# Kernel tuning notes

Hardware: AMD Instinct MI355X
Metric: run time of the kernel (lower is better)

Reference implementation:

```python
import jax, jax.numpy as jnp
import numpy as np

N, D, H, OUT, B = 100000, 512, 1024, 250, 256
EPS = 1e-5


def layernorm(x, g, b):
    m = jnp.mean(x, axis=-1, keepdims=True)
    v = jnp.mean(jnp.square(x - m), axis=-1, keepdims=True)
    return (x - m) * jax.lax.rsqrt(v + EPS) * g + b


def setup_inputs() -> dict:
    key = jax.random.key(0)
    ks = jax.random.split(key, 10)
    s = lambda fan: (2.0 / fan) ** 0.5  # kaiming-ish scale
    return {
        "x": jax.random.normal(ks[0], (N, D), jnp.float32),
        "batch_ids": jnp.sort(jax.random.randint(ks[1], (N,), 0, B)),
        "gW1": jax.random.normal(ks[2], (2 * D, D), jnp.float32) * s(D),
        "gb1": jnp.zeros((2 * D,), jnp.float32),
        "gln_g": jnp.ones((2 * D,), jnp.float32),
        "gln_b": jnp.zeros((2 * D,), jnp.float32),
        "gW2": jax.random.normal(ks[3], (1, 2 * D), jnp.float32) * s(2 * D),
        "gb2": jnp.zeros((1,), jnp.float32),
        "pn_g": jnp.ones((D,), jnp.float32),
        "pn_b": jnp.zeros((D,), jnp.float32),
        "mW1": jax.random.normal(ks[4], (H, D), jnp.float32) * s(D),
        "mb1": jnp.zeros((H,), jnp.float32),
        "mln_g": jnp.ones((H,), jnp.float32),
        "mln_b": jnp.zeros((H,), jnp.float32),
        "mW2": jax.random.normal(ks[5], (OUT, H), jnp.float32) * s(H),
        "mb2": jnp.zeros((OUT,), jnp.float32),
    }


def reference(x, batch_ids, gW1, gb1, gln_g, gln_b, gW2, gb2,
              pn_g, pn_b, mW1, mb1, mln_g, mln_b, mW2, mb2):
    # gate MLP: Linear -> LayerNorm -> ReLU -> Linear(->1)
    h = jax.nn.relu(layernorm(x @ gW1.T + gb1, gln_g, gln_b))  # [N, 2D]
    gate = (h @ gW2.T + gb2)[:, 0]                              # [N]
    # segment-wise softmax over batch_ids
    seg_max = jax.ops.segment_max(gate, batch_ids, num_segments=B)
    e = jnp.exp(gate - jax.lax.stop_gradient(seg_max)[batch_ids])
    denom = jax.ops.segment_sum(e, batch_ids, num_segments=B)
    w = e / denom[batch_ids]                                    # [N]
    pooled = jax.ops.segment_sum(w[:, None] * x, batch_ids, num_segments=B)  # [B, D]
    out = layernorm(pooled, pn_g, pn_b)
    # classifier MLP (dropout = identity in eval)
    z = jax.nn.relu(layernorm(out @ mW1.T + mb1, mln_g, mln_b))
    logits = z @ mW2.T + mb2                                    # [B, OUT]
    return logits
```

## Files before the change

### kernel.cpp

```cpp
#include <hip/hip_runtime.h>
#include <stdint.h>

typedef unsigned int u32;
typedef unsigned short u16;

#define NROWS 100000
#define DIM 512
#define HDIM 1024
#define OUTF 250
#define NSEG 256
#define LNEPS 1e-5f
#define BM 32
#define NG 3125

typedef __bf16 bf16_t;
typedef bf16_t bf16x4 __attribute__((ext_vector_type(4)));
typedef bf16_t bf16x8 __attribute__((ext_vector_type(8)));
typedef float f32x4 __attribute__((ext_vector_type(4)));

__device__ inline int lower_bound(const int* __restrict__ a, int n, int v) {
    int lo = 0, hi = n;
    while (lo < hi) {
        int m = (lo + hi) >> 1;
        if (a[m] < v) lo = m + 1; else hi = m;
    }
    return lo;
}

__global__ __launch_bounds__(256) void k_conv(const float* __restrict__ gW1,
                                              const float* __restrict__ mW1,
                                              const float* __restrict__ mW2,
                                              u16* __restrict__ Wf,
                                              u16* __restrict__ mW1f,
                                              u16* __restrict__ mW2f) {
    int bid = blockIdx.x;
    if (bid < 512) {
        const float* src_base = (bid < 256) ? gW1 : mW1;
        u16* dst = (bid < 256) ? Wf : mW1f;
        int gid  = (bid & 255) * 256 + threadIdx.x;
        int lane = gid & 63;
        int grp  = gid >> 6;
        int ks   = grp >> 6, nt = grp & 63;
        int n    = nt * 16 + (lane & 15);
        int k0   = ks * 32 + ((lane >> 4) << 3);
        const float* src = src_base + (size_t)n * DIM + k0;
        float4 f0 = *reinterpret_cast<const float4*>(src);
        float4 f1 = *reinterpret_cast<const float4*>(src + 4);
        bf16x8 v;
        v[0] = (bf16_t)f0.x; v[1] = (bf16_t)f0.y;
        v[2] = (bf16_t)f0.z; v[3] = (bf16_t)f0.w;
        v[4] = (bf16_t)f1.x; v[5] = (bf16_t)f1.y;
        v[6] = (bf16_t)f1.z; v[7] = (bf16_t)f1.w;
        reinterpret_cast<bf16x8*>(dst)[gid] = v;
    } else {
        int gid  = (bid - 512) * 256 + threadIdx.x;
        int lane = gid & 63;
        int grp  = gid >> 6;
        int ks   = grp >> 4, nt = grp & 15;
        int n    = nt * 16 + (lane & 15);
        int k0   = ks * 32 + ((lane >> 4) << 3);
        bf16x8 v;
        if (n < OUTF) {
            const float* src = mW2 + (size_t)n * HDIM + k0;
            float4 f0 = *reinterpret_cast<const float4*>(src);
            float4 f1 = *reinterpret_cast<const float4*>(src + 4);
            v[0] = (bf16_t)f0.x; v[1] = (bf16_t)f0.y;
            v[2] = (bf16_t)f0.z; v[3] = (bf16_t)f0.w;
            v[4] = (bf16_t)f1.x; v[5] = (bf16_t)f1.y;
            v[6] = (bf16_t)f1.z; v[7] = (bf16_t)f1.w;
        } else {
            #pragma unroll
            for (int j = 0; j < 8; ++j) v[j] = (bf16_t)0.f;
        }
        reinterpret_cast<bf16x8*>(mW2f)[gid] = v;
    }
}

__global__ __launch_bounds__(512) void k_gate(
    const float* __restrict__ x, const u16* __restrict__ Wf,
    const float* __restrict__ gb1,
    const float* __restrict__ gln_g, const float* __restrict__ gln_b,
    const float* __restrict__ gW2, const float* __restrict__ gb2,
    float* __restrict__ gate)
{
    __shared__ __align__(16) u16 xlds[BM * DIM];
    __shared__ float redS[8][BM];
    __shared__ float redQ[8][BM];
    __shared__ float meanA[BM], rstdA[BM];

    const int tid  = threadIdx.x;
    const int lane = tid & 63;
    const int w    = tid >> 6;
    const int l15  = lane & 15;
    const int g4   = lane >> 4;
    const int row0 = blockIdx.x * BM;

    #pragma unroll
    for (int uu = 0; uu < 4; ++uu) {
        int lu  = uu * 512 + tid;
        int r   = lu >> 6;
        int u   = lu & 63;
        const float* src = x + (size_t)(row0 + r) * DIM + (u << 3);
        float4 f0 = *reinterpret_cast<const float4*>(src);
        float4 f1 = *reinterpret_cast<const float4*>(src + 4);
        bf16x8 v;
        v[0] = (bf16_t)f0.x; v[1] = (bf16_t)f0.y;
        v[2] = (bf16_t)f0.z; v[3] = (bf16_t)f0.w;
        v[4] = (bf16_t)f1.x; v[5] = (bf16_t)f1.y;
        v[6] = (bf16_t)f1.z; v[7] = (bf16_t)f1.w;
        int phys = r * DIM + ((u ^ (r & 7)) << 3);
        *reinterpret_cast<bf16x8*>(&xlds[phys]) = v;
    }
    __syncthreads();

    f32x4 acc[2][8];
    #pragma unroll
    for (int m = 0; m < 2; ++m)
        #pragma unroll
        for (int t = 0; t < 8; ++t)
            acc[m][t] = (f32x4){0.f, 0.f, 0.f, 0.f};

    const bf16x8* __restrict__ WfB = reinterpret_cast<const bf16x8*>(Wf);

    auto loadB = [&](bf16x8 (&b)[8], int ks) {
        #pragma unroll
        for (int t = 0; t < 8; ++t)
            b[t] = WfB[(ks * 64 + w * 8 + t) * 64 + lane];
    };
    auto loadA = [&](bf16x8 (&a)[2], int ks) {
        #pragma unroll
        for (int m = 0; m < 2; ++m) {
            int r = m * 16 + l15;
            int u = ks * 4 + g4;
            a[m] = *reinterpret_cast<const bf16x8*>(&xlds[r * DIM + ((u ^ (r & 7)) << 3)]);
        }
    };
    auto domfma = [&](bf16x8 (&a)[2], bf16x8 (&b)[8]) {
        #pragma unroll
        for (int m = 0; m < 2; ++m)
            #pragma unroll
            for (int t = 0; t < 8; ++t)
                acc[m][t] = __builtin_amdgcn_mfma_f32_16x16x32_bf16(a[m], b[t], acc[m][t], 0, 0, 0);
    };

    bf16x8 b0[8], b1[8], a0[2], a1[2];
    loadB(b0, 0); loadA(a0, 0);
    #pragma unroll
    for (int ks2 = 0; ks2 < 8; ++ks2) {
        loadB(b1, 2 * ks2 + 1);
        loadA(a1, 2 * ks2 + 1);
        domfma(a0, b0);
        if (ks2 < 7) {
            loadB(b0, 2 * ks2 + 2);
            loadA(a0, 2 * ks2 + 2);
        }
        domfma(a1, b1);
    }

    float cbias[8];
    #pragma unroll
    for (int t = 0; t < 8; ++t) cbias[t] = gb1[(w * 8 + t) * 16 + l15];
    #pragma unroll
    for (int m = 0; m < 2; ++m)
        #pragma unroll
        for (int t = 0; t < 8; ++t)
            #pragma unroll
            for (int j = 0; j < 4; ++j)
                acc[m][t][j] += cbias[t];

    #pragma unroll
    for (int m = 0; m < 2; ++m) {
        #pragma unroll
        for (int j = 0; j < 4; ++j) {
            float s1 = 0.f, s2 = 0.f;
            #pragma unroll
            for (int t = 0; t < 8; ++t) {
                float v = acc[m][t][j];
                s1 += v; s2 += v * v;
            }
            #pragma unroll
            for (int off = 1; off < 16; off <<= 1) {
                s1 += __shfl_xor(s1, off);
                s2 += __shfl_xor(s2, off);
            }
            if (l15 == 0) {
                int row = m * 16 + g4 * 4 + j;
                redS[w][row] = s1;
                redQ[w][row] = s2;
            }
        }
    }
    __syncthreads();
    if (tid < BM) {
        float S1 = 0.f, S2 = 0.f;
        #pragma unroll
        for (int ww = 0; ww < 8; ++ww) { S1 += redS[ww][tid]; S2 += redQ[ww][tid]; }
        float mean = S1 * (1.0f / 1024.0f);
        float var  = S2 * (1.0f / 1024.0f) - mean * mean;
        meanA[tid] = mean;
        rstdA[tid] = rsqrtf(var + LNEPS);
    }
    __syncthreads();

    float cg[8], cb[8], cw[8];
    #pragma unroll
    for (int t = 0; t < 8; ++t) {
        int c = (w * 8 + t) * 16 + l15;
        cg[t] = gln_g[c]; cb[t] = gln_b[c]; cw[t] = gW2[c];
    }
    #pragma unroll
    for (int m = 0; m < 2; ++m) {
        #pragma unroll
        for (int j = 0; j < 4; ++j) {
            int row = m * 16 + g4 * 4 + j;
            float mn = meanA[row];
            float rs = rstdA[row];
            float gp = 0.f;
            #pragma unroll
            for (int t = 0; t < 8; ++t) {
                float h = (acc[m][t][j] - mn) * rs * cg[t] + cb[t];
                gp += fmaxf(h, 0.f) * cw[t];
            }
            #pragma unroll
            for (int off = 1; off < 16; off <<= 1)
                gp += __shfl_xor(gp, off);
            if (l15 == 0) redS[w][row] = gp;
        }
    }
    __syncthreads();
    if (tid < BM) {
        float s = gb2[0];
        #pragma unroll
        for (int ww = 0; ww < 8; ++ww) s += redS[ww][tid];
        gate[row0 + tid] = s;
    }
}

__global__ __launch_bounds__(256) void k_seg(const int* __restrict__ ids,
                                             const float* __restrict__ gate,
                                             float* __restrict__ segmax,
                                             float* __restrict__ segden) {
    int b = blockIdx.x, tid = threadIdx.x;
    int start = lower_bound(ids, NROWS, b);
    int end   = lower_bound(ids, NROWS, b + 1);
    __shared__ float sh[4];

    float lm = -INFINITY;
    for (int i = start + tid; i < end; i += 256) lm = fmaxf(lm, gate[i]);
    #pragma unroll
    for (int off = 32; off; off >>= 1) lm = fmaxf(lm, __shfl_xor(lm, off));
    if ((tid & 63) == 0) sh[tid >> 6] = lm;
    __syncthreads();
    float m = fmaxf(fmaxf(sh[0], sh[1]), fmaxf(sh[2], sh[3]));
    __syncthreads();

    float ls = 0.f;
    for (int i = start + tid; i < end; i += 256) ls += __expf(gate[i] - m);
    #pragma unroll
    for (int off = 32; off; off >>= 1) ls += __shfl_xor(ls, off);
    if ((tid & 63) == 0) sh[tid >> 6] = ls;
    __syncthreads();
    if (tid == 0) {
        segmax[b] = m;
        segden[b] = sh[0] + sh[1] + sh[2] + sh[3];
    }
}

__global__ __launch_bounds__(512) void k_poolp(const int* __restrict__ ids,
                                               const float* __restrict__ gate,
                                               const float* __restrict__ x,
                                               const float* __restrict__ segmax,
                                               const float* __restrict__ segden,
                                               float* __restrict__ pooledp) {
    const int b = blockIdx.x, q = blockIdx.y, tid = threadIdx.x;
    const int slot   = tid & 127;
    const int stripe = tid >> 7;
    const int start = lower_bound(ids, NROWS, b);
    const int end   = lower_bound(ids, NROWS, b + 1);
    const float m   = segmax[b];
    const float den = segden[b];
    const float inv = (den > 0.f) ? 1.0f / den : 0.0f;

    __shared__ f32x4 sh[4][128];

    const f32x4* __restrict__ xr = reinterpret_cast<const f32x4*>(x);
    f32x4 acc = (f32x4){0.f, 0.f, 0.f, 0.f};
    for (int i = start + q * 4 + stripe; i < end; i += 16) {
        float wgt = __expf(gate[i] - m) * inv;
        f32x4 xv = xr[(size_t)i * 128 + slot];
        acc += wgt * xv;
    }
    sh[stripe][slot] = acc;
    __syncthreads();
    if (tid < 128) {
        f32x4 r = sh[0][tid] + sh[1][tid] + sh[2][tid] + sh[3][tid];
        reinterpret_cast<f32x4*>(pooledp)[(q * NSEG + b) * 128 + tid] = r;
    }
}

__global__ __launch_bounds__(128) void k_pln(const float* __restrict__ pooledp,
                                             const float* __restrict__ pn_g,
                                             const float* __restrict__ pn_b,
                                             u16* __restrict__ outbf) {
    const int b = blockIdx.x, tid = threadIdx.x;
    const f32x4* pp = reinterpret_cast<const f32x4*>(pooledp);
    f32x4 v = pp[(0 * NSEG + b) * 128 + tid] + pp[(1 * NSEG + b) * 128 + tid]
            + pp[(2 * NSEG + b) * 128 + tid] + pp[(3 * NSEG + b) * 128 + tid];
    float s = v[0] + v[1] + v[2] + v[3];
    float q = v[0]*v[0] + v[1]*v[1] + v[2]*v[2] + v[3]*v[3];
    #pragma unroll
    for (int off = 32; off; off >>= 1) {
        s += __shfl_xor(s, off);
        q += __shfl_xor(q, off);
    }
    __shared__ float sh[4];
    if ((tid & 63) == 0) { sh[(tid >> 6) * 2] = s; sh[(tid >> 6) * 2 + 1] = q; }
    __syncthreads();
    float S = sh[0] + sh[2], Q = sh[1] + sh[3];
    float mean = S * (1.0f / 512.0f);
    float rstd = rsqrtf(Q * (1.0f / 512.0f) - mean * mean + LNEPS);
    f32x4 g = reinterpret_cast<const f32x4*>(pn_g)[tid];
    f32x4 bb = reinterpret_cast<const f32x4*>(pn_b)[tid];
    bf16x4 o;
    #pragma unroll
    for (int j = 0; j < 4; ++j)
        o[j] = (bf16_t)((v[j] - mean) * rstd * g[j] + bb[j]);
    reinterpret_cast<bf16x4*>(outbf)[b * 128 + tid] = o;
}

__global__ __launch_bounds__(512) void k_heady(const u16* __restrict__ outbf,
                                               const u16* __restrict__ mW1f,
                                               const float* __restrict__ mb1,
                                               float* __restrict__ y) {
    __shared__ __align__(16) u16 alds[128 * DIM];
    const int tid  = threadIdx.x;
    const int lane = tid & 63;
    const int w    = tid >> 6;
    const int wm   = w >> 2;
    const int wn   = w & 3;
    const int l15  = lane & 15;
    const int g4   = lane >> 4;
    const int hc   = blockIdx.x;
    const int sh_  = blockIdx.y;

    const uint4* srcU = reinterpret_cast<const uint4*>(outbf);
    #pragma unroll
    for (int uu = 0; uu < 16; ++uu) {
        int lu = uu * 512 + tid;
        int r  = lu >> 6;
        int u  = lu & 63;
        uint4 val = srcU[(size_t)(sh_ * 128 + r) * 64 + u];
        int phys = r * DIM + ((u ^ (r & 7)) << 3);
        *reinterpret_cast<uint4*>(&alds[phys]) = val;
    }
    __syncthreads();

    f32x4 acc[4][4];
    #pragma unroll
    for (int m = 0; m < 4; ++m)
        #pragma unroll
        for (int t = 0; t < 4; ++t)
            acc[m][t] = (f32x4){0.f, 0.f, 0.f, 0.f};

    const bf16x8* __restrict__ WB = reinterpret_cast<const bf16x8*>(mW1f);
    #pragma unroll 4
    for (int ks = 0; ks < 16; ++ks) {
        bf16x8 b[4];
        #pragma unroll
        for (int t = 0; t < 4; ++t) {
            int nt_g = hc * 16 + wn * 4 + t;
            b[t] = WB[(ks * 64 + nt_g) * 64 + lane];
        }
        bf16x8 a[4];
        #pragma unroll
        for (int m = 0; m < 4; ++m) {
            int r = wm * 64 + m * 16 + l15;
            int u = ks * 4 + g4;
            a[m] = *reinterpret_cast<const bf16x8*>(&alds[r * DIM + ((u ^ (r & 7)) << 3)]);
        }
        #pragma unroll
        for (int m = 0; m < 4; ++m)
            #pragma unroll
            for (int t = 0; t < 4; ++t)
                acc[m][t] = __builtin_amdgcn_mfma_f32_16x16x32_bf16(a[m], b[t], acc[m][t], 0, 0, 0);
    }

    #pragma unroll
    for (int t = 0; t < 4; ++t) {
        int col = hc * 256 + (wn * 4 + t) * 16 + l15;
        float bias = mb1[col];
        #pragma unroll
        for (int m = 0; m < 4; ++m)
            #pragma unroll
            for (int j = 0; j < 4; ++j) {
                int seg = sh_ * 128 + wm * 64 + m * 16 + g4 * 4 + j;
                y[(size_t)seg * HDIM + col] = acc[m][t][j] + bias;
            }
    }
}

__global__ __launch_bounds__(256) void k_headz(const float* __restrict__ y,
                                               const float* __restrict__ mln_g,
                                               const float* __restrict__ mln_b,
                                               u16* __restrict__ zbf) {
    const int b = blockIdx.x, tid = threadIdx.x;
    f32x4 v = reinterpret_cast<const f32x4*>(y)[b * 256 + tid];
    float s = v[0] + v[1] + v[2] + v[3];
    float q = v[0]*v[0] + v[1]*v[1] + v[2]*v[2] + v[3]*v[3];
    #pragma unroll
    for (int off = 32; off; off >>= 1) {
        s += __shfl_xor(s, off);
        q += __shfl_xor(q, off);
    }
    __shared__ float sh[8];
    if ((tid & 63) == 0) { sh[(tid >> 6) * 2] = s; sh[(tid >> 6) * 2 + 1] = q; }
    __syncthreads();
    float S = sh[0] + sh[2] + sh[4] + sh[6];
    float Q = sh[1] + sh[3] + sh[5] + sh[7];
    float mean = S * (1.0f / 1024.0f);
    float rstd = rsqrtf(Q * (1.0f / 1024.0f) - mean * mean + LNEPS);
    f32x4 g = reinterpret_cast<const f32x4*>(mln_g)[tid];
    f32x4 bb = reinterpret_cast<const f32x4*>(mln_b)[tid];
    bf16x4 o;
    #pragma unroll
    for (int j = 0; j < 4; ++j)
        o[j] = (bf16_t)fmaxf((v[j] - mean) * rstd * g[j] + bb[j], 0.f);
    reinterpret_cast<bf16x4*>(zbf)[b * 256 + tid] = o;
}

__global__ __launch_bounds__(512) void k_logits(const u16* __restrict__ zbf,
                                                const u16* __restrict__ mW2f,
                                                const float* __restrict__ mb2,
                                                float* __restrict__ logits) {
    __shared__ __align__(16) u16 alds[128 * 256];
    const int tid  = threadIdx.x;
    const int lane = tid & 63;
    const int w    = tid >> 6;
    const int wm   = w >> 2;
    const int wn   = w & 3;
    const int l15  = lane & 15;
    const int g4   = lane >> 4;
    const int sh_  = blockIdx.x;

    f32x4 acc[4][4];
    #pragma unroll
    for (int m = 0; m < 4; ++m)
        #pragma unroll
        for (int t = 0; t < 4; ++t)
            acc[m][t] = (f32x4){0.f, 0.f, 0.f, 0.f};

    const uint4* srcU = reinterpret_cast<const uint4*>(zbf);
    const bf16x8* __restrict__ WB = reinterpret_cast<const bf16x8*>(mW2f);

    for (int kc = 0; kc < 4; ++kc) {
        __syncthreads();
        #pragma unroll
        for (int uu = 0; uu < 8; ++uu) {
            int lu = uu * 512 + tid;
            int r  = lu >> 5;
            int u  = lu & 31;
            uint4 val = srcU[(size_t)(sh_ * 128 + r) * 128 + kc * 32 + u];
            int phys = r * 256 + ((u ^ (r & 7)) << 3);
            *reinterpret_cast<uint4*>(&alds[phys]) = val;
        }
        __syncthreads();
        #pragma unroll
        for (int ksl = 0; ksl < 8; ++ksl) {
            bf16x8 b[4];
            #pragma unroll
            for (int t = 0; t < 4; ++t)
                b[t] = WB[((kc * 8 + ksl) * 16 + wn * 4 + t) * 64 + lane];
            bf16x8 a[4];
            #pragma unroll
            for (int m = 0; m < 4; ++m) {
                int r = wm * 64 + m * 16 + l15;
                int u = ksl * 4 + g4;
                a[m] = *reinterpret_cast<const bf16x8*>(&alds[r * 256 + ((u ^ (r & 7)) << 3)]);
            }
            #pragma unroll
            for (int m = 0; m < 4; ++m)
                #pragma unroll
                for (int t = 0; t < 4; ++t)
                    acc[m][t] = __builtin_amdgcn_mfma_f32_16x16x32_bf16(a[m], b[t], acc[m][t], 0, 0, 0);
        }
    }

    #pragma unroll
    for (int t = 0; t < 4; ++t) {
        int col = (wn * 4 + t) * 16 + l15;
        if (col < OUTF) {
            float bias = mb2[col];
            #pragma unroll
            for (int m = 0; m < 4; ++m)
                #pragma unroll
                for (int j = 0; j < 4; ++j) {
                    int seg = sh_ * 128 + wm * 64 + m * 16 + g4 * 4 + j;
                    logits[(size_t)seg * OUTF + col] = acc[m][t][j] + bias;
                }
        }
    }
}

extern "C" void kernel_launch(void* const* d_in, const int* in_sizes, int n_in,
                              void* d_out, int out_size, void* d_ws, size_t ws_size,
                              hipStream_t stream) {
    const float* x     = (const float*)d_in[0];
    const int*   ids   = (const int*)  d_in[1];
    const float* gW1   = (const float*)d_in[2];
    const float* gb1   = (const float*)d_in[3];
    const float* gln_g = (const float*)d_in[4];
    const float* gln_b = (const float*)d_in[5];
    const float* gW2   = (const float*)d_in[6];
    const float* gb2   = (const float*)d_in[7];
    const float* pn_g  = (const float*)d_in[8];
    const float* pn_b  = (const float*)d_in[9];
    const float* mW1   = (const float*)d_in[10];
    const float* mb1   = (const float*)d_in[11];
    const float* mln_g = (const float*)d_in[12];
    const float* mln_b = (const float*)d_in[13];
    const float* mW2   = (const float*)d_in[14];
    const float* mb2   = (const float*)d_in[15];
    float* logits = (float*)d_out;

    char* ws = (char*)d_ws;
    const size_t MB = 1 << 20;
    u16*   Wf      = (u16*)  (ws);
    u16*   mW1f    = (u16*)  (ws + 1 * MB);
    u16*   mW2f    = (u16*)  (ws + 2 * MB);
    float* gate    = (float*)(ws + 5 * MB / 2);
    float* segmax  = (float*)(ws + 3 * MB);
    float* segden  = segmax + NSEG;
    float* pooledp = (float*)(ws + 4 * MB);
    u16*   outbf   = (u16*)  (ws + 6 * MB);
    float* y       = (float*)(ws + 7 * MB);
    u16*   zbf     = (u16*)  (ws + 8 * MB);

    hipLaunchKernelGGL(k_conv, dim3(640), dim3(256), 0, stream,
                       gW1, mW1, mW2, Wf, mW1f, mW2f);
    hipLaunchKernelGGL(k_gate, dim3(NG), dim3(512), 0, stream,
                       x, Wf, gb1, gln_g, gln_b, gW2, gb2, gate);
    hipLaunchKernelGGL(k_seg, dim3(NSEG), dim3(256), 0, stream,
                       ids, gate, segmax, segden);
    hipLaunchKernelGGL(k_poolp, dim3(NSEG, 4), dim3(512), 0, stream,
                       ids, gate, x, segmax, segden, pooledp);
    hipLaunchKernelGGL(k_pln, dim3(NSEG), dim3(128), 0, stream,
                       pooledp, pn_g, pn_b, outbf);
    hipLaunchKernelGGL(k_heady, dim3(4, 2), dim3(512), 0, stream,
                       outbf, mW1f, mb1, y);
    hipLaunchKernelGGL(k_headz, dim3(NSEG), dim3(256), 0, stream,
                       y, mln_g, mln_b, zbf);
    hipLaunchKernelGGL(k_logits, dim3(2), dim3(512), 0, stream,
                       zbf, mW2f, mb2, logits);
}
```

Baseline: 245.7 us.

## Pre-convert x to swizzled bf16 and make gate kernel persistent with async LDS staging

```diff
diff --git a/kernel.cpp b/kernel.cpp
--- a/kernel.cpp
+++ b/kernel.cpp
@@ -10,13 +10,16 @@
 #define OUTF 250
 #define NSEG 256
 #define LNEPS 1e-5f
-#define BM 32
-#define NG 3125
+#define BM 64
+#define NT 1563
+#define GATE_GRID 256
 
 typedef __bf16 bf16_t;
 typedef bf16_t bf16x4 __attribute__((ext_vector_type(4)));
 typedef bf16_t bf16x8 __attribute__((ext_vector_type(8)));
 typedef float f32x4 __attribute__((ext_vector_type(4)));
+
+#define BAR_LGKM() asm volatile("s_waitcnt lgkmcnt(0)\n\ts_barrier" ::: "memory")
 
 __device__ inline int lower_bound(const int* __restrict__ a, int n, int v) {
     int lo = 0, hi = n;
@@ -30,9 +33,11 @@
 __global__ __launch_bounds__(256) void k_conv(const float* __restrict__ gW1,
                                               const float* __restrict__ mW1,
                                               const float* __restrict__ mW2,
+                                              const float* __restrict__ x,
                                               u16* __restrict__ Wf,
                                               u16* __restrict__ mW1f,
-                                              u16* __restrict__ mW2f) {
+                                              u16* __restrict__ mW2f,
+                                              u16* __restrict__ xbf) {
     int bid = blockIdx.x;
     if (bid < 512) {
         const float* src_base = (bid < 256) ? gW1 : mW1;
@@ -52,7 +57,7 @@
         v[4] = (bf16_t)f1.x; v[5] = (bf16_t)f1.y;
         v[6] = (bf16_t)f1.z; v[7] = (bf16_t)f1.w;
         reinterpret_cast<bf16x8*>(dst)[gid] = v;
-    } else {
+    } else if (bid < 640) {
         int gid  = (bid - 512) * 256 + threadIdx.x;
         int lane = gid & 63;
         int grp  = gid >> 6;
@@ -73,19 +78,38 @@
             for (int j = 0; j < 8; ++j) v[j] = (bf16_t)0.f;
         }
         reinterpret_cast<bf16x8*>(mW2f)[gid] = v;
-    }
-}
-
-__global__ __launch_bounds__(512) void k_gate(
-    const float* __restrict__ x, const u16* __restrict__ Wf,
+    } else {
+        int gid = (bid - 640) * 256 + threadIdx.x;
+        int i   = gid >> 6;
+        int up  = gid & 63;
+        bf16x8 v;
+        if (i < NROWS) {
+            int u = up ^ (i & 7);
+            const float* src = x + (size_t)i * DIM + (u << 3);
+            float4 f0 = *reinterpret_cast<const float4*>(src);
+            float4 f1 = *reinterpret_cast<const float4*>(src + 4);
+            v[0] = (bf16_t)f0.x; v[1] = (bf16_t)f0.y;
+            v[2] = (bf16_t)f0.z; v[3] = (bf16_t)f0.w;
+            v[4] = (bf16_t)f1.x; v[5] = (bf16_t)f1.y;
+            v[6] = (bf16_t)f1.z; v[7] = (bf16_t)f1.w;
+        } else {
+            #pragma unroll
+            for (int j = 0; j < 8; ++j) v[j] = (bf16_t)0.f;
+        }
+        reinterpret_cast<bf16x8*>(xbf)[gid] = v;
+    }
+}
+
+__global__ __launch_bounds__(1024, 4) void k_gate(
+    const u16* __restrict__ xbf, const u16* __restrict__ Wf,
     const float* __restrict__ gb1,
     const float* __restrict__ gln_g, const float* __restrict__ gln_b,
     const float* __restrict__ gW2, const float* __restrict__ gb2,
     float* __restrict__ gate)
 {
-    __shared__ __align__(16) u16 xlds[BM * DIM];
-    __shared__ float redS[8][BM];
-    __shared__ float redQ[8][BM];
+    __shared__ __align__(16) u16 xlds[2][BM * DIM];
+    __shared__ float redS[16][BM];
+    __shared__ float redQ[16][BM];
     __shared__ float meanA[BM], rstdA[BM];
 
     const int tid  = threadIdx.x;
@@ -93,146 +117,143 @@
     const int w    = tid >> 6;
     const int l15  = lane & 15;
     const int g4   = lane >> 4;
-    const int row0 = blockIdx.x * BM;
-
-    #pragma unroll
-    for (int uu = 0; uu < 4; ++uu) {
-        int lu  = uu * 512 + tid;
-        int r   = lu >> 6;
-        int u   = lu & 63;
-        const float* src = x + (size_t)(row0 + r) * DIM + (u << 3);
-        float4 f0 = *reinterpret_cast<const float4*>(src);
-        float4 f1 = *reinterpret_cast<const float4*>(src + 4);
-        bf16x8 v;
-        v[0] = (bf16_t)f0.x; v[1] = (bf16_t)f0.y;
-        v[2] = (bf16_t)f0.z; v[3] = (bf16_t)f0.w;
-        v[4] = (bf16_t)f1.x; v[5] = (bf16_t)f1.y;
-        v[6] = (bf16_t)f1.z; v[7] = (bf16_t)f1.w;
-        int phys = r * DIM + ((u ^ (r & 7)) << 3);
-        *reinterpret_cast<bf16x8*>(&xlds[phys]) = v;
-    }
-    __syncthreads();
-
-    f32x4 acc[2][8];
-    #pragma unroll
-    for (int m = 0; m < 2; ++m)
-        #pragma unroll
-        for (int t = 0; t < 8; ++t)
-            acc[m][t] = (f32x4){0.f, 0.f, 0.f, 0.f};
 
     const bf16x8* __restrict__ WfB = reinterpret_cast<const bf16x8*>(Wf);
-
-    auto loadB = [&](bf16x8 (&b)[8], int ks) {
-        #pragma unroll
-        for (int t = 0; t < 8; ++t)
-            b[t] = WfB[(ks * 64 + w * 8 + t) * 64 + lane];
+    const float gb2v = gb2[0];
+
+    auto stage = [&](int t, int buf) {
+        #pragma unroll
+        for (int uu = 0; uu < 4; ++uu) {
+            const u16* gp = xbf + ((size_t)t * 4096 + uu * 1024 + tid) * 8;
+            u16* lp = &xlds[buf][(uu * 1024 + w * 64) * 8];
+            __builtin_amdgcn_global_load_lds(
+                (const __attribute__((address_space(1))) u32*)gp,
+                (__attribute__((address_space(3))) u32*)lp, 16, 0, 0);
+        }
     };
-    auto loadA = [&](bf16x8 (&a)[2], int ks) {
-        #pragma unroll
-        for (int m = 0; m < 2; ++m) {
-            int r = m * 16 + l15;
-            int u = ks * 4 + g4;
-            a[m] = *reinterpret_cast<const bf16x8*>(&xlds[r * DIM + ((u ^ (r & 7)) << 3)]);
-        }
-    };
-    auto domfma = [&](bf16x8 (&a)[2], bf16x8 (&b)[8]) {
-        #pragma unroll
-        for (int m = 0; m < 2; ++m)
-            #pragma unroll
-            for (int t = 0; t < 8; ++t)
-                acc[m][t] = __builtin_amdgcn_mfma_f32_16x16x32_bf16(a[m], b[t], acc[m][t], 0, 0, 0);
-    };
-
-    bf16x8 b0[8], b1[8], a0[2], a1[2];
-    loadB(b0, 0); loadA(a0, 0);
-    #pragma unroll
-    for (int ks2 = 0; ks2 < 8; ++ks2) {
-        loadB(b1, 2 * ks2 + 1);
-        loadA(a1, 2 * ks2 + 1);
-        domfma(a0, b0);
-        if (ks2 < 7) {
-            loadB(b0, 2 * ks2 + 2);
-            loadA(a0, 2 * ks2 + 2);
-        }
-        domfma(a1, b1);
-    }
-
-    float cbias[8];
-    #pragma unroll
-    for (int t = 0; t < 8; ++t) cbias[t] = gb1[(w * 8 + t) * 16 + l15];
-    #pragma unroll
-    for (int m = 0; m < 2; ++m)
-        #pragma unroll
-        for (int t = 0; t < 8; ++t)
-            #pragma unroll
-            for (int j = 0; j < 4; ++j)
-                acc[m][t][j] += cbias[t];
-
-    #pragma unroll
-    for (int m = 0; m < 2; ++m) {
-        #pragma unroll
-        for (int j = 0; j < 4; ++j) {
-            float s1 = 0.f, s2 = 0.f;
-            #pragma unroll
-            for (int t = 0; t < 8; ++t) {
-                float v = acc[m][t][j];
-                s1 += v; s2 += v * v;
+
+    stage(blockIdx.x, 0);
+    int cur = 0;
+    for (int t = blockIdx.x; t < NT; t += GATE_GRID) {
+        __syncthreads();
+        const u16* xl = xlds[cur];
+
+        f32x4 acc[4][4];
+        #pragma unroll
+        for (int m = 0; m < 4; ++m)
+            #pragma unroll
+            for (int t4 = 0; t4 < 4; ++t4)
+                acc[m][t4] = (f32x4){0.f, 0.f, 0.f, 0.f};
+
+        auto loadB = [&](bf16x8 (&b)[4], int ks) {
+            #pragma unroll
+            for (int t4 = 0; t4 < 4; ++t4)
+                b[t4] = WfB[(ks * 64 + w * 4 + t4) * 64 + lane];
+        };
+        auto step = [&](bf16x8 (&b)[4], int ks) {
+            bf16x8 a[4];
+            #pragma unroll
+            for (int m = 0; m < 4; ++m) {
+                int r = m * 16 + l15;
+                int u = ks * 4 + g4;
+                a[m] = *reinterpret_cast<const bf16x8*>(&xl[r * DIM + ((u ^ (r & 7)) << 3)]);
             }
             #pragma unroll
-            for (int off = 1; off < 16; off <<= 1) {
-                s1 += __shfl_xor(s1, off);
-                s2 += __shfl_xor(s2, off);
+            for (int m = 0; m < 4; ++m)
+                #pragma unroll
+                for (int t4 = 0; t4 < 4; ++t4)
+                    acc[m][t4] = __builtin_amdgcn_mfma_f32_16x16x32_bf16(a[m], b[t4], acc[m][t4], 0, 0, 0);
+        };
+
+        bf16x8 b0[4], b1[4];
+        loadB(b0, 0);
+        #pragma unroll
+        for (int ks2 = 0; ks2 < 8; ++ks2) {
+            loadB(b1, 2 * ks2 + 1);
+            step(b0, 2 * ks2);
+            if (ks2 < 7) loadB(b0, 2 * ks2 + 2);
+            step(b1, 2 * ks2 + 1);
+        }
+
+        float cbias[4], cg[4], cb[4], cw[4];
+        #pragma unroll
+        for (int t4 = 0; t4 < 4; ++t4) {
+            int c = (w * 4 + t4) * 16 + l15;
+            cbias[t4] = gb1[c]; cg[t4] = gln_g[c]; cb[t4] = gln_b[c]; cw[t4] = gW2[c];
+        }
+        __builtin_amdgcn_sched_barrier(0);
+        if (t + GATE_GRID < NT) stage(t + GATE_GRID, cur ^ 1);
+
+        #pragma unroll
+        for (int m = 0; m < 4; ++m)
+            #pragma unroll
+            for (int t4 = 0; t4 < 4; ++t4)
+                #pragma unroll
+                for (int j = 0; j < 4; ++j)
+                    acc[m][t4][j] += cbias[t4];
+
+        #pragma unroll
+        for (int m = 0; m < 4; ++m) {
+            #pragma unroll
+            for (int j = 0; j < 4; ++j) {
+                float s1 = 0.f, s2 = 0.f;
+                #pragma unroll
+                for (int t4 = 0; t4 < 4; ++t4) {
+                    float v = acc[m][t4][j];
+                    s1 += v; s2 += v * v;
+                }
+                #pragma unroll
+                for (int off = 1; off < 16; off <<= 1) {
+                    s1 += __shfl_xor(s1, off);
+                    s2 += __shfl_xor(s2, off);
+                }
+                if (l15 == 0) {
+                    int row = m * 16 + g4 * 4 + j;
+                    redS[w][row] = s1;
+                    redQ[w][row] = s2;
+                }
             }
-            if (l15 == 0) {
+        }
+        BAR_LGKM();
+        if (tid < BM) {
+            float S1 = 0.f, S2 = 0.f;
+            #pragma unroll
+            for (int ww = 0; ww < 16; ++ww) { S1 += redS[ww][tid]; S2 += redQ[ww][tid]; }
+            float mean = S1 * (1.0f / 1024.0f);
+            float var  = S2 * (1.0f / 1024.0f) - mean * mean;
+            meanA[tid] = mean;
+            rstdA[tid] = rsqrtf(var + LNEPS);
+        }
+        BAR_LGKM();
+
+        #pragma unroll
+        for (int m = 0; m < 4; ++m) {
+            #pragma unroll
+            for (int j = 0; j < 4; ++j) {
                 int row = m * 16 + g4 * 4 + j;
-                redS[w][row] = s1;
-                redQ[w][row] = s2;
+                float mn = meanA[row];
+                float rs = rstdA[row];
+                float gp = 0.f;
+                #pragma unroll
+                for (int t4 = 0; t4 < 4; ++t4) {
+                    float h = (acc[m][t4][j] - mn) * rs * cg[t4] + cb[t4];
+                    gp += fmaxf(h, 0.f) * cw[t4];
+                }
+                #pragma unroll
+                for (int off = 1; off < 16; off <<= 1)
+                    gp += __shfl_xor(gp, off);
+                if (l15 == 0) redS[w][row] = gp;
             }
         }
-    }
-    __syncthreads();
-    if (tid < BM) {
-        float S1 = 0.f, S2 = 0.f;
-        #pragma unroll
-        for (int ww = 0; ww < 8; ++ww) { S1 += redS[ww][tid]; S2 += redQ[ww][tid]; }
-        float mean = S1 * (1.0f / 1024.0f);
-        float var  = S2 * (1.0f / 1024.0f) - mean * mean;
-        meanA[tid] = mean;
-        rstdA[tid] = rsqrtf(var + LNEPS);
-    }
-    __syncthreads();
-
-    float cg[8], cb[8], cw[8];
-    #pragma unroll
-    for (int t = 0; t < 8; ++t) {
-        int c = (w * 8 + t) * 16 + l15;
-        cg[t] = gln_g[c]; cb[t] = gln_b[c]; cw[t] = gW2[c];
-    }
-    #pragma unroll
-    for (int m = 0; m < 2; ++m) {
-        #pragma unroll
-        for (int j = 0; j < 4; ++j) {
-            int row = m * 16 + g4 * 4 + j;
-            float mn = meanA[row];
-            float rs = rstdA[row];
-            float gp = 0.f;
-            #pragma unroll
-            for (int t = 0; t < 8; ++t) {
-                float h = (acc[m][t][j] - mn) * rs * cg[t] + cb[t];
-                gp += fmaxf(h, 0.f) * cw[t];
-            }
-            #pragma unroll
-            for (int off = 1; off < 16; off <<= 1)
-                gp += __shfl_xor(gp, off);
-            if (l15 == 0) redS[w][row] = gp;
-        }
-    }
-    __syncthreads();
-    if (tid < BM) {
-        float s = gb2[0];
-        #pragma unroll
-        for (int ww = 0; ww < 8; ++ww) s += redS[ww][tid];
-        gate[row0 + tid] = s;
+        BAR_LGKM();
+        if (tid < BM) {
+            float s = gb2v;
+            #pragma unroll
+            for (int ww = 0; ww < 16; ++ww) s += redS[ww][tid];
+            int row = t * 64 + tid;
+            if (row < NROWS) gate[row] = s;
+        }
+        cur ^= 1;
     }
 }
 
@@ -268,33 +289,40 @@
 
 __global__ __launch_bounds__(512) void k_poolp(const int* __restrict__ ids,
                                                const float* __restrict__ gate,
-                                               const float* __restrict__ x,
+                                               const u16* __restrict__ xbf,
                                                const float* __restrict__ segmax,
                                                const float* __restrict__ segden,
                                                float* __restrict__ pooledp) {
     const int b = blockIdx.x, q = blockIdx.y, tid = threadIdx.x;
-    const int slot   = tid & 127;
-    const int stripe = tid >> 7;
+    const int s      = tid & 63;
+    const int stripe = tid >> 6;
     const int start = lower_bound(ids, NROWS, b);
     const int end   = lower_bound(ids, NROWS, b + 1);
     const float m   = segmax[b];
     const float den = segden[b];
     const float inv = (den > 0.f) ? 1.0f / den : 0.0f;
 
-    __shared__ f32x4 sh[4][128];
-
-    const f32x4* __restrict__ xr = reinterpret_cast<const f32x4*>(x);
-    f32x4 acc = (f32x4){0.f, 0.f, 0.f, 0.f};
-    for (int i = start + q * 4 + stripe; i < end; i += 16) {
+    float acc[8];
+    #pragma unroll
+    for (int j = 0; j < 8; ++j) acc[j] = 0.f;
+
+    for (int i = start + q * 8 + stripe; i < end; i += 32) {
         float wgt = __expf(gate[i] - m) * inv;
-        f32x4 xv = xr[(size_t)i * 128 + slot];
-        acc += wgt * xv;
-    }
-    sh[stripe][slot] = acc;
-    __syncthreads();
-    if (tid < 128) {
-        f32x4 r = sh[0][tid] + sh[1][tid] + sh[2][tid] + sh[3][tid];
-        reinterpret_cast<f32x4*>(pooledp)[(q * NSEG + b) * 128 + tid] = r;
+        bf16x8 xv = *reinterpret_cast<const bf16x8*>(xbf + ((size_t)i * 64 + (s ^ (i & 7))) * 8);
+        #pragma unroll
+        for (int j = 0; j < 8; ++j) acc[j] += wgt * (float)xv[j];
+    }
+
+    __shared__ float sh[8][64][8];
+    #pragma unroll
+    for (int j = 0; j < 8; ++j) sh[stripe][s][j] = acc[j];
+    __syncthreads();
+    {
+        int u = tid >> 3, j = tid & 7;
+        float r = 0.f;
+        #pragma unroll
+        for (int st = 0; st < 8; ++st) r += sh[st][u][j];
+        pooledp[((size_t)q * NSEG + b) * DIM + u * 8 + j] = r;
     }
 }
 
@@ -534,15 +562,16 @@
     u16*   outbf   = (u16*)  (ws + 6 * MB);
     float* y       = (float*)(ws + 7 * MB);
     u16*   zbf     = (u16*)  (ws + 8 * MB);
-
-    hipLaunchKernelGGL(k_conv, dim3(640), dim3(256), 0, stream,
-                       gW1, mW1, mW2, Wf, mW1f, mW2f);
-    hipLaunchKernelGGL(k_gate, dim3(NG), dim3(512), 0, stream,
-                       x, Wf, gb1, gln_g, gln_b, gW2, gb2, gate);
+    u16*   xbf     = (u16*)  (ws + 16 * MB);
+
+    hipLaunchKernelGGL(k_conv, dim3(640 + 25008), dim3(256), 0, stream,
+                       gW1, mW1, mW2, x, Wf, mW1f, mW2f, xbf);
+    hipLaunchKernelGGL(k_gate, dim3(GATE_GRID), dim3(1024), 0, stream,
+                       xbf, Wf, gb1, gln_g, gln_b, gW2, gb2, gate);
     hipLaunchKernelGGL(k_seg, dim3(NSEG), dim3(256), 0, stream,
                        ids, gate, segmax, segden);
     hipLaunchKernelGGL(k_poolp, dim3(NSEG, 4), dim3(512), 0, stream,
-                       ids, gate, x, segmax, segden, pooledp);
+                       ids, gate, xbf, segmax, segden, pooledp);
     hipLaunchKernelGGL(k_pln, dim3(NSEG), dim3(128), 0, stream,
                        pooledp, pn_g, pn_b, outbf);
     hipLaunchKernelGGL(k_heady, dim3(4, 2), dim3(512), 0, stream,
```

Measured after the change: 672.5 us. 174% more time.
